# Kernel tuning notes

Measured on AMD Instinct MI355X. Metric: run time of the kernel, lower is better.

The kernel has to match this reference:

```python
import jax, jax.numpy as jnp
import numpy as np

B, S, N_CATE, N_CONT = 32, 1024, 4, 4
HIDDEN, ATTN, VOCAB, EMB = 1024, 512, 1000, 128


def sinusoidal_pe(seq_len, d_model, base=10000.0):
    pos = jnp.arange(seq_len, dtype=jnp.float32)[:, None]            # [S,1]
    i = jnp.arange(d_model // 2, dtype=jnp.float32)[None, :]         # [1,D/2]
    ang = pos / jnp.power(base, 2.0 * i / d_model)                   # [S,D/2]
    pe = jnp.zeros((seq_len, d_model), dtype=jnp.float32)
    pe = pe.at[:, 0::2].set(jnp.sin(ang))
    pe = pe.at[:, 1::2].set(jnp.cos(ang))
    return pe


def setup_inputs() -> dict:
    key = jax.random.key(0)
    ks = jax.random.split(key, 20)
    s = 0.02
    inp = {
        "cate_x": jax.random.randint(ks[0], (B, S, N_CATE), 0, VOCAB, dtype=jnp.int64)
                  if jax.config.read("jax_enable_x64") else
                  jax.random.randint(ks[0], (B, S, N_CATE), 0, VOCAB, dtype=jnp.int32),
        "cont_x": jax.random.normal(ks[1], (B, S, N_CONT), dtype=jnp.float32),
        "mask": jnp.ones((B, S), dtype=bool),
        "targets": jax.random.uniform(ks[2], (B, S), dtype=jnp.float32),
        # EntireEmbedding params: 4 cate tables + cont linear + comb projection
        "E0": jax.random.normal(ks[3], (VOCAB, EMB), dtype=jnp.float32) * s,
        "E1": jax.random.normal(ks[4], (VOCAB, EMB), dtype=jnp.float32) * s,
        "E2": jax.random.normal(ks[5], (VOCAB, EMB), dtype=jnp.float32) * s,
        "E3": jax.random.normal(ks[6], (VOCAB, EMB), dtype=jnp.float32) * s,
        "Wc": jax.random.normal(ks[7], (N_CONT, N_CATE * EMB), dtype=jnp.float32) * s,
        "Wproj": jax.random.normal(ks[8], (2 * N_CATE * EMB, HIDDEN), dtype=jnp.float32) * s,
        # two-head attention linears (bias=False)
        "WQ1": jax.random.normal(ks[9], (HIDDEN, ATTN), dtype=jnp.float32) * s,
        "WK1": jax.random.normal(ks[10], (HIDDEN, ATTN), dtype=jnp.float32) * s,
        "WV1": jax.random.normal(ks[11], (HIDDEN, ATTN), dtype=jnp.float32) * s,
        "WQ2": jax.random.normal(ks[12], (HIDDEN, ATTN), dtype=jnp.float32) * s,
        "WK2": jax.random.normal(ks[13], (HIDDEN, ATTN), dtype=jnp.float32) * s,
        "WV2": jax.random.normal(ks[14], (HIDDEN, ATTN), dtype=jnp.float32) * s,
        "W0": jax.random.normal(ks[15], (2 * ATTN, HIDDEN), dtype=jnp.float32) * s,
        "Wf": jax.random.normal(ks[16], (HIDDEN, 1), dtype=jnp.float32) * s,
    }
    return inp


def _attend(x, WQ, WK, WV):
    Q = x @ WQ  # [B,S,A]
    K = x @ WK
    V = x @ WV
    scores = jnp.einsum("bqd,bkd->bqk", Q, K) / jnp.sqrt(jnp.float32(ATTN))
    # faithful to nn.Softmax(dim=1): normalize over the QUERY axis
    attn = jax.nn.softmax(scores, axis=1)
    return jnp.einsum("bqk,bkv->bqv", attn, V)


def reference(cate_x, cont_x, mask, targets, E0, E1, E2, E3, Wc, Wproj,
              WQ1, WK1, WV1, WQ2, WK2, WV2, W0, Wf):
    # EntireEmbedding: per-feature cate embeddings + cont projection -> comb proj
    cate_emb = jnp.concatenate(
        [E0[cate_x[..., 0]], E1[cate_x[..., 1]], E2[cate_x[..., 2]], E3[cate_x[..., 3]]],
        axis=-1)                                   # [B,S,512]
    cont_emb = cont_x @ Wc                          # [B,S,512]
    x = jnp.concatenate([cate_emb, cont_emb], axis=-1) @ Wproj  # [B,S,H]
    x = x + sinusoidal_pe(x.shape[1], HIDDEN)[None, :, :]
    z1 = _attend(x, WQ1, WK1, WV1)                  # [B,S,A]
    z2 = _attend(x, WQ2, WK2, WV2)                  # [B,S,A]
    z = jnp.concatenate([z1, z2], axis=-1) @ W0     # [B,S,H]
    out = jax.nn.sigmoid(z @ Wf)                    # FinalConnecting: Linear(H,1)+sigmoid
    return out.squeeze(-1)                          # [B,S]
```

## Files before the change

kernel.cpp:

```cpp
#include <hip/hip_runtime.h>
#include <hip/hip_bf16.h>
#include <math.h>

#define BB    32
#define SS    1024
#define HID   1024
#define AT    512
#define NVOC  1000
#define NT    (BB*SS)

typedef unsigned short u16;
typedef __attribute__((ext_vector_type(8))) short s16x8;
typedef __attribute__((ext_vector_type(4))) float f32x4;

__device__ __forceinline__ float bf2f(u16 u) {
    union { unsigned int i; float f; } x; x.i = ((unsigned int)u) << 16; return x.f;
}
__device__ __forceinline__ u16 f2bf(float f) {
    union { float f; unsigned int i; } u; u.f = f;
    unsigned int r = u.i + 0x7fffu + ((u.i >> 16) & 1u);
    return (u16)(r >> 16);
}
__device__ __forceinline__ float4 ld4(const float* p) { return *(const float4*)p; }
__device__ __forceinline__ float4 ld4bf(const u16* p) {
    ushort4 v = *(const ushort4*)p;
    return make_float4(bf2f(v.x), bf2f(v.y), bf2f(v.z), bf2f(v.w));
}

__device__ __forceinline__ void gld16(const u16* g, u16* l) {
    __builtin_amdgcn_global_load_lds(
        (const __attribute__((address_space(1))) unsigned int*)g,
        (__attribute__((address_space(3))) unsigned int*)l,
        16, 0, 0);
}

struct Ptrs4f { const float* p[4]; };

__device__ __forceinline__ float blockReduceSum(float x) {
    #pragma unroll
    for (int off = 32; off > 0; off >>= 1) x += __shfl_down(x, off, 64);
    __shared__ float tmp[4];
    int lane = threadIdx.x & 63, wid = threadIdx.x >> 6;
    if (lane == 0) tmp[wid] = x;
    __syncthreads();
    if (threadIdx.x == 0) x = tmp[0] + tmp[1] + tmp[2] + tmp[3];
    return x;
}
__device__ __forceinline__ float waveReduceSum(float x) {
    #pragma unroll
    for (int off = 32; off > 0; off >>= 1) x += __shfl_down(x, off, 64);
    return x;
}

__global__ void k_prep(Ptrs4f E, const float* __restrict__ Wproj,
                       u16* __restrict__ PE16, u16* __restrict__ E16o, u16* __restrict__ Wp16) {
    int blk = blockIdx.x, tid = threadIdx.x;
    if (blk < 2048) {
        int idx = blk*256 + tid;
        int s = idx >> 9, i = idx & 511;
        const float l2_10000 = 13.287712379549449f;
        float denom = exp2f((2.f * (float)i / 1024.f) * l2_10000);
        float ang = (float)s / denom;
        unsigned int pack = ((unsigned int)f2bf(cosf(ang)) << 16) | f2bf(sinf(ang));
        *(unsigned int*)(PE16 + (size_t)s*1024 + 2*i) = pack;
    } else if (blk < 4048) {
        int id2 = blk - 2048;
        int f = id2 / 500;
        int i = (id2 % 500)*256 + tid;
        E16o[(size_t)f*128000 + i] = f2bf(E.p[f][i]);
    } else {
        int i = (blk - 4048)*256 + tid;
        Wp16[i] = f2bf(Wproj[i]);
    }
}

__global__ void k_transp(Ptrs4f src, u16* __restrict__ dst, int R, int C) {
    const float* in = src.p[blockIdx.z];
    u16* out = dst + (size_t)blockIdx.z * R * C;
    int r0 = blockIdx.y*32, c0 = blockIdx.x*32;
    __shared__ float tt[32][33];
    tt[threadIdx.y][threadIdx.x] = in[(size_t)(r0 + threadIdx.y)*C + c0 + threadIdx.x];
    __syncthreads();
    out[(size_t)(c0 + threadIdx.y)*R + r0 + threadIdx.x] = f2bf(tt[threadIdx.x][threadIdx.y]);
}

__global__ void k_pre1(const float* __restrict__ W0, const float* __restrict__ Wf,
                       const float* __restrict__ Wc, const float* __restrict__ Wproj,
                       float* __restrict__ W0f, float* __restrict__ Wcp, float* __restrict__ CQ) {
    int blk = blockIdx.x, tid = threadIdx.x;
    if (blk < 1024) {
        const float* row = W0 + (size_t)blk*1024;
        float a = 0.f;
        for (int j = tid; j < 1024; j += 256) a += row[j] * Wf[j];
        a = blockReduceSum(a);
        if (tid == 0) W0f[blk] = a;
    } else if (blk < 1040) {
        int r = blk - 1024; int c = r >> 2, is = r & 3; int i = is*256 + tid;
        float a = 0.f;
        for (int j = 0; j < 512; ++j) a += Wc[c*512 + j] * Wproj[(size_t)(512 + j)*1024 + i];
        Wcp[c*1024 + i] = a;
    } else {
        int r = blk - 1040;
        CQ[r*256 + tid] = 0.f;
    }
}

__global__ void k_pre2(Ptrs4f W, const float* __restrict__ WV1, const float* __restrict__ WV2,
                       const float* __restrict__ W0f, const float* __restrict__ Wcp,
                       float* __restrict__ v, float* __restrict__ CQ) {
    int blk = blockIdx.x, tid = threadIdx.x;
    if (blk < 2048) {
        int h = blk >> 10, i = blk & 1023;
        const float* WV = h ? WV2 : WV1;
        const float* wf = W0f + h*512;
        float a = 0.f;
        for (int aa = tid; aa < 512; aa += 256) a += WV[(size_t)i*512 + aa] * wf[aa];
        a = blockReduceSum(a);
        if (tid == 0) v[h*1024 + i] = a;
    } else {
        int r = blk - 2048;
        int ns = r & 1, wc = (r >> 1) & 15, jc = r >> 5;
        int w = wc & 3, c = wc >> 2; int n = ns*256 + tid;
        const float* Ww = W.p[w];
        float a = 0.f;
        for (int j = jc*128; j < jc*128 + 128; ++j) a += Wcp[c*1024 + j] * Ww[(size_t)j*512 + n];
        atomicAdd(&CQ[(size_t)(w*4 + c)*512 + n], a);
    }
}

__device__ __forceinline__ void cstore(float* p, float v) { *p = v; }
__device__ __forceinline__ void cstore(u16* p, float v)   { *p = f2bf(v); }

template<typename CT, bool STATS, bool CTRANS>
__device__ __forceinline__ void mfma_gemm(const u16* __restrict__ A, const u16* __restrict__ B,
                                          CT* __restrict__ C, int M, int N, int K, float alpha,
                                          float* __restrict__ Pm, float* __restrict__ Pd,
                                          int m0, int n0) {
    __shared__ u16 As[128*64];
    __shared__ u16 Bs[128*64];
    const int tid = threadIdx.x;
    const int wave = tid >> 6, lane = tid & 63;
    const int quad = lane >> 4, l16 = lane & 15;
    const int wm = (wave >> 1)*64, wn = (wave & 1)*64;
    const int srow = lane >> 3;
    const int scol = ((lane & 7) ^ srow) * 8;
    f32x4 acc[4][4] = {};

    for (int k0 = 0; k0 < K; k0 += 64) {
        #pragma unroll
        for (int p = 0; p < 4; ++p) {
            int rb = wave*32 + p*8;
            gld16(A + (size_t)(m0 + rb + srow)*K + k0 + scol, As + rb*64);
            gld16(B + (size_t)(n0 + rb + srow)*K + k0 + scol, Bs + rb*64);
        }
        __syncthreads();
        #pragma unroll
        for (int kk = 0; kk < 2; ++kk) {
            s16x8 af[4], bf[4];
            #pragma unroll
            for (int i = 0; i < 4; ++i) {
                int row = wm + i*16 + l16;
                af[i] = *(const s16x8*)(As + row*64 + (((kk*4 + quad) ^ (row & 7)) * 8));
            }
            #pragma unroll
            for (int j = 0; j < 4; ++j) {
                int row = wn + j*16 + l16;
                bf[j] = *(const s16x8*)(Bs + row*64 + (((kk*4 + quad) ^ (row & 7)) * 8));
            }
            #pragma unroll
            for (int i = 0; i < 4; ++i)
                #pragma unroll
                for (int j = 0; j < 4; ++j)
                    acc[i][j] = __builtin_amdgcn_mfma_f32_16x16x32_bf16(af[i], bf[j], acc[i][j], 0, 0, 0);
        }
        __syncthreads();
    }
    if (STATS) {
        #pragma unroll
        for (int i = 0; i < 4; ++i)
            #pragma unroll
            for (int r = 0; r < 4; ++r) {
                int gm = m0 + wm + i*16 + quad*4 + r;
                u16 b0 = f2bf(acc[i][0][r] * alpha);
                u16 b1 = f2bf(acc[i][1][r] * alpha);
                u16 b2 = f2bf(acc[i][2][r] * alpha);
                u16 b3 = f2bf(acc[i][3][r] * alpha);
                acc[i][0][r] = bf2f(b0); acc[i][1][r] = bf2f(b1);
                acc[i][2][r] = bf2f(b2); acc[i][3][r] = bf2f(b3);
                unsigned int lo = (unsigned int)b0 | ((unsigned int)b1 << 16);
                unsigned int hi = (unsigned int)b2 | ((unsigned int)b3 << 16);
                *(uint2*)((u16*)C + (size_t)gm*N + n0 + wn + l16*4) = make_uint2(lo, hi);
            }
        __shared__ float sMax[4][64];
        __shared__ float sSum[4][64];
        #pragma unroll
        for (int j = 0; j < 4; ++j) {
            float mx = -3.4e38f;
            #pragma unroll
            for (int i = 0; i < 4; ++i)
                #pragma unroll
                for (int r = 0; r < 4; ++r) mx = fmaxf(mx, acc[i][j][r]);
            mx = fmaxf(mx, __shfl_xor(mx, 16, 64));
            mx = fmaxf(mx, __shfl_xor(mx, 32, 64));
            float sm = 0.f;
            #pragma unroll
            for (int i = 0; i < 4; ++i)
                #pragma unroll
                for (int r = 0; r < 4; ++r) sm += exp2f(acc[i][j][r] - mx);
            sm += __shfl_xor(sm, 16, 64);
            sm += __shfl_xor(sm, 32, 64);
            if (quad == 0) { sMax[wave][j*16 + l16] = mx; sSum[wave][j*16 + l16] = sm; }
        }
        __syncthreads();
        if (tid < 128) {
            int c = tid;
            int w0 = (c < 64) ? 0 : 1, ci = c & 63;
            float m0v = sMax[w0][ci],     s0 = sSum[w0][ci];
            float m1v = sMax[w0 + 2][ci], s1 = sSum[w0 + 2][ci];
            float mm = fmaxf(m0v, m1v);
            float ss = s0 * exp2f(m0v - mm) + s1 * exp2f(m1v - mm);
            Pm[n0 + c] = mm;
            Pd[n0 + c] = ss;
        }
    } else {
        #pragma unroll
        for (int i = 0; i < 4; ++i) {
            #pragma unroll
            for (int r = 0; r < 4; ++r) {
                int gm = m0 + wm + i*16 + quad*4 + r;
                if (gm < M) {
                    #pragma unroll
                    for (int j = 0; j < 4; ++j) {
                        int gn = n0 + wn + j*16 + l16;
                        if (CTRANS) cstore(C + (size_t)gn*M + gm, acc[i][j][r] * alpha);
                        else        cstore(C + (size_t)gm*N + gn, acc[i][j][r] * alpha);
                    }
                }
            }
        }
    }
}

__global__ __launch_bounds__(256) void k_pw_pre3(const u16* __restrict__ Wp16, const u16* __restrict__ Wt,
                                                 u16* __restrict__ PWT,
                                                 const float* __restrict__ Wproj, const float* __restrict__ v,
                                                 float* __restrict__ pv) {
    int blk = blockIdx.x;
    if (blk < 64) {
        int x = blk & 3, z = blk >> 2;
        int f = z >> 2, w = z & 3;
        mfma_gemm<u16,false,true>(Wp16 + (size_t)f*128*1024, Wt + (size_t)w*512*1024,
                                  PWT + (size_t)z*512*128, 128, 512, 1024, 1.f,
                                  nullptr, nullptr, 0, x*128);
    } else {
        int b2 = blk - 64, tid = threadIdx.x;
        int i = b2 & 127, fh = b2 >> 7; int f = fh >> 1, h = fh & 1;
        const float* row = Wproj + (size_t)(f*128 + i)*1024;
        const float* vh = v + h*1024;
        float a = 0.f;
        for (int j = tid; j < 1024; j += 256) a += row[j] * vh[j];
        a = blockReduceSum(a);
        if (tid == 0) pv[(size_t)fh*128 + i] = a;
    }
}

__global__ __launch_bounds__(256) void k_g_TP(const u16* __restrict__ E16, const u16* __restrict__ PWT,
                                              const u16* __restrict__ PE16, const u16* __restrict__ Wt,
                                              u16* __restrict__ TQK16, u16* __restrict__ PEQ16) {
    int z = blockIdx.z;
    if (z < 16) {
        int f = z >> 2;
        mfma_gemm<u16,false,false>(E16 + (size_t)f*128000, PWT + (size_t)z*512*128,
                   TQK16 + (size_t)z*1000*512, 1000, 512, 128, 1.f, nullptr, nullptr,
                   blockIdx.y*128, blockIdx.x*128);
    } else {
        int w = z - 16;
        mfma_gemm<u16,false,false>(PE16, Wt + (size_t)w*512*1024, PEQ16 + (size_t)w*1024*512,
                   1024, 512, 1024, 1.f, nullptr, nullptr, blockIdx.y*128, blockIdx.x*128);
    }
}

__global__ __launch_bounds__(256, 6) void k_g_S(const u16* __restrict__ Q, const u16* __restrict__ K,
                                             u16* __restrict__ Sb, float alpha,
                                             float* __restrict__ Pm, float* __restrict__ Pd, int b0) {
    size_t b = blockIdx.z;
    int bx = (blockIdx.x % 4)*2 + (blockIdx.y % 2);
    int by = (blockIdx.x / 4)*4 + (blockIdx.y / 2);
    size_t po = ((b0 + b)*8 + by)*1024;
    mfma_gemm<u16,true,false>(Q + b*SS*AT, K + b*SS*AT, Sb + b*SS*SS, 1024, 1024, 512, alpha,
                        Pm + po, Pd + po, by*128, bx*128);
}

__global__ void k_dots(const u16* __restrict__ E16, const u16* __restrict__ PE16,
                       const float* __restrict__ Wcp, const float* __restrict__ v,
                       const float* __restrict__ pv,
                       float* __restrict__ Ut, float* __restrict__ pu, float* __restrict__ cu) {
    int id = blockIdx.x;
    if (id < 2000) {
        int wave = threadIdx.x >> 6, lane = threadIdx.x & 63;
        int d = id*4 + wave;
        int f = d / 2000, h = (d / 1000) & 1, r = d % 1000;
        unsigned int e2 = *(const unsigned int*)(E16 + ((size_t)f*1000 + r)*128 + lane*2);
        const float* pvp = pv + (size_t)(f*2 + h)*128 + lane*2;
        float a = bf2f((u16)(e2 & 0xffff)) * pvp[0] + bf2f((u16)(e2 >> 16)) * pvp[1];
        a = waveReduceSum(a);
        if (lane == 0) Ut[(size_t)(f*2 + h)*1000 + r] = a;
    } else if (id < 4048) {
        int tq = id - 2000; int h = tq >> 10, s = tq & 1023;
        float4 a = ld4bf(PE16 + (size_t)s*1024 + threadIdx.x*4);
        float4 b = ld4(v + h*1024 + threadIdx.x*4);
        float p = a.x*b.x + a.y*b.y + a.z*b.z + a.w*b.w;
        p = blockReduceSum(p);
        if (threadIdx.x == 0) pu[h*1024 + s] = p;
    } else {
        int tq = id - 4048; int h = tq >> 2, c = tq & 3;
        float4 a = ld4(Wcp + c*1024 + threadIdx.x*4);
        float4 b = ld4(v + h*1024 + threadIdx.x*4);
        float p = a.x*b.x + a.y*b.y + a.z*b.z + a.w*b.w;
        p = blockReduceSum(p);
        if (threadIdx.x == 0) cu[h*4 + c] = p;
    }
}

__device__ __forceinline__ void unpack8(uint4 v, float* x) {
    x[0] = bf2f((u16)(v.x & 0xffff)); x[1] = bf2f((u16)(v.x >> 16));
    x[2] = bf2f((u16)(v.y & 0xffff)); x[3] = bf2f((u16)(v.y >> 16));
    x[4] = bf2f((u16)(v.z & 0xffff)); x[5] = bf2f((u16)(v.z >> 16));
    x[6] = bf2f((u16)(v.w & 0xffff)); x[7] = bf2f((u16)(v.w >> 16));
}

__global__ void k_gather(const int* __restrict__ cate, const float* __restrict__ cont,
                         const u16* __restrict__ TQK, const float* __restrict__ CQ,
                         const u16* __restrict__ PEQ, const float* __restrict__ Ut,
                         const float* __restrict__ cu, const float* __restrict__ pu,
                         u16* __restrict__ Qh, u16* __restrict__ Kh,
                         float* __restrict__ u, int h) {
    int tid = threadIdx.x;
    size_t t = (size_t)blockIdx.x*2 + (tid >> 7);
    int r = tid & 127;
    int s = (int)(t & 1023);
    int4 cc = *(const int4*)(cate + t*4);
    float4 cv = ld4(cont + t*4);
    int e = r >> 6;
    int w = 2*h + e;
    int n = (r & 63)*8;
    const u16* t0 = TQK + ((size_t)(0*4  + w)*1000 + cc.x)*512 + n;
    const u16* t1 = TQK + ((size_t)(1*4  + w)*1000 + cc.y)*512 + n;
    const u16* t2 = TQK + ((size_t)(2*4  + w)*1000 + cc.z)*512 + n;
    const u16* t3 = TQK + ((size_t)(3*4  + w)*1000 + cc.w)*512 + n;
    const u16* pq = PEQ + ((size_t)w*1024 + s)*512 + n;
    const float* cq = CQ + (size_t)w*2048 + n;
    float a0[8], a1[8], a2[8], a3[8], ap[8];
    unpack8(*(const uint4*)t0, a0); unpack8(*(const uint4*)t1, a1);
    unpack8(*(const uint4*)t2, a2); unpack8(*(const uint4*)t3, a3);
    unpack8(*(const uint4*)pq, ap);
    unsigned int pack[4];
    #pragma unroll
    for (int jp = 0; jp < 4; ++jp) {
        float x0, x1;
        #pragma unroll
        for (int half = 0; half < 2; ++half) {
            int j = jp*2 + half;
            float x = a0[j] + a1[j] + a2[j] + a3[j] + ap[j]
                    + cv.x*cq[j] + cv.y*cq[512+j] + cv.z*cq[1024+j] + cv.w*cq[1536+j];
            if (half == 0) x0 = x; else x1 = x;
        }
        pack[jp] = ((unsigned int)f2bf(x1) << 16) | f2bf(x0);
    }
    u16* op = (e ? Kh : Qh) + t*512 + n;
    *(uint4*)op = make_uint4(pack[0], pack[1], pack[2], pack[3]);
    if (r == 0) {
        float uu = pu[h*1024 + s]
                 + Ut[(0*2 + h)*1000 + cc.x] + Ut[(1*2 + h)*1000 + cc.y]
                 + Ut[(2*2 + h)*1000 + cc.z] + Ut[(3*2 + h)*1000 + cc.w]
                 + cv.x*cu[h*4+0] + cv.y*cu[h*4+1] + cv.z*cu[h*4+2] + cv.w*cu[h*4+3];
        u[(size_t)h*NT + t] = uu;
    }
}

__global__ void k_stats_combine(const float* __restrict__ Pm, const float* __restrict__ Pd,
                                const float* __restrict__ u, float* __restrict__ wexp, int b0) {
    int idx = b0*1024 + blockIdx.x*256 + threadIdx.x;
    int b = idx >> 10, k = idx & 1023;
    float mx = -3.4e38f;
    #pragma unroll
    for (int mt = 0; mt < 8; ++mt) mx = fmaxf(mx, Pm[((size_t)b*8 + mt)*1024 + k]);
    float dd = 0.f;
    #pragma unroll
    for (int mt = 0; mt < 8; ++mt) dd += Pd[((size_t)b*8 + mt)*1024 + k]
                                       * exp2f(Pm[((size_t)b*8 + mt)*1024 + k] - mx);
    int q = (k & ~63) | (((k & 15) << 2) | ((k & 63) >> 4));
    wexp[((size_t)b << 10) + q] = u[idx] / dd * exp2f(-mx);
}

__global__ void k_logit(const u16* __restrict__ Sb, const float* __restrict__ wexp,
                        float* __restrict__ logits, int b0, int init) {
    int wave = threadIdx.x >> 6, lane = threadIdx.x & 63;
    size_t tl = (size_t)blockIdx.x*4 + wave;
    size_t tabs = (size_t)b0*1024 + tl;
    int b = (int)(tabs >> 10);
    const u16* row = Sb + tl*1024;
    const float* wb = wexp + ((size_t)b << 10);
    float acc = 0.f;
    #pragma unroll
    for (int half = 0; half < 2; ++half) {
        int k = lane*8 + half*512;
        float4 s0 = ld4bf(row + k), s1 = ld4bf(row + k + 4);
        float4 w0 = ld4(wb + k),    w1 = ld4(wb + k + 4);
        acc += exp2f(s0.x)*w0.x + exp2f(s0.y)*w0.y + exp2f(s0.z)*w0.z + exp2f(s0.w)*w0.w
             + exp2f(s1.x)*w1.x + exp2f(s1.y)*w1.y + exp2f(s1.z)*w1.z + exp2f(s1.w)*w1.w;
    }
    acc = waveReduceSum(acc);
    if (lane == 0) { if (init) logits[tabs] = acc; else logits[tabs] += acc; }
}

__global__ void k_final(const float* __restrict__ logits, float* __restrict__ out) {
    int t = blockIdx.x*256 + threadIdx.x;
    float x = logits[t];
    out[t] = 1.f / (1.f + expf(-x));
}

extern "C" void kernel_launch(void* const* d_in, const int* in_sizes, int n_in,
                              void* d_out, int out_size, void* d_ws, size_t ws_size,
                              hipStream_t stream) {
    const int*   cate = (const int*)d_in[0];
    const float* cont = (const float*)d_in[1];
    Ptrs4f E; E.p[0] = (const float*)d_in[4]; E.p[1] = (const float*)d_in[5];
              E.p[2] = (const float*)d_in[6]; E.p[3] = (const float*)d_in[7];
    const float* Wc    = (const float*)d_in[8];
    const float* Wproj = (const float*)d_in[9];
    Ptrs4f W; W.p[0] = (const float*)d_in[10];
              W.p[1] = (const float*)d_in[11];
              W.p[2] = (const float*)d_in[13];
              W.p[3] = (const float*)d_in[14];
    const float* WV1 = (const float*)d_in[12];
    const float* WV2 = (const float*)d_in[15];
    const float* W0  = (const float*)d_in[16];
    const float* Wf  = (const float*)d_in[17];

    char* base = (char*)d_ws;
    size_t off = 0;
    auto alloc = [&](size_t bytes) { void* p = base + off; off += (bytes + 255) & ~(size_t)255; return p; };
    u16*   PE16  = (u16*)  alloc(1048576ull*2);
    u16*   E16   = (u16*)  alloc(4ull*1000*128*2);
    u16*   Wt    = (u16*)  alloc(4ull*512*1024*2);
    u16*   Wp16  = (u16*)  alloc(512ull*1024*2);
    u16*   PWT   = (u16*)  alloc(16ull*512*128*2);
    u16*   TQK16 = (u16*)  alloc(16ull*1000*512*2);
    u16*   PEQ16 = (u16*)  alloc(4ull*1024*512*2);
    float* Wcp   = (float*)alloc(4*1024*4);
    float* W0f   = (float*)alloc(1024*4);
    float* vv    = (float*)alloc(2*1024*4);
    float* CQ    = (float*)alloc(16*512*4);
    float* pvb   = (float*)alloc(8*128*4);
    float* Ut    = (float*)alloc(8*1000*4);
    float* cu    = (float*)alloc(8*4);
    float* pu    = (float*)alloc(2*1024*4);
    float* ubuf  = (float*)alloc(2ull*NT*4);
    u16*   Qh    = (u16*)  alloc((size_t)NT*512*2);
    u16*   Kh    = (u16*)  alloc((size_t)NT*512*2);
    float* Pm    = (float*)alloc(32ull*8*1024*4);
    float* Pd    = (float*)alloc(32ull*8*1024*4);
    float* wbuf  = (float*)alloc(32*1024*4);
    float* logits= (float*)alloc((size_t)NT*4);
    size_t sChunkBytes = (size_t)SS*SS*2;
    size_t remain = (ws_size > off) ? (ws_size - off) : 0;
    int NB = (int)(remain / sChunkBytes);
    if (NB > 32) NB = 32;
    if (NB < 1) NB = 1;
    u16* Sbuf = (u16*)(base + off);

    const float alpha = 0.06375954951107036f;

    k_prep<<<6096, 256, 0, stream>>>(E, Wproj, PE16, E16, Wp16);
    k_transp<<<dim3(16, 32, 4), dim3(32, 32), 0, stream>>>(W, Wt, 1024, 512);
    k_pre1<<<1072, 256, 0, stream>>>(W0, Wf, Wc, Wproj, W0f, Wcp, CQ);
    k_pre2<<<2304, 256, 0, stream>>>(W, WV1, WV2, W0f, Wcp, vv, CQ);
    k_pw_pre3<<<1088, 256, 0, stream>>>(Wp16, Wt, PWT, Wproj, vv, pvb);
    k_g_TP<<<dim3(4, 8, 20), 256, 0, stream>>>(E16, PWT, PE16, Wt, TQK16, PEQ16);
    k_dots<<<4056, 256, 0, stream>>>(E16, PE16, Wcp, vv, pvb, Ut, pu, cu);

    for (int h = 0; h < 2; ++h) {
        k_gather<<<NT/2, 256, 0, stream>>>(cate, cont, TQK16, CQ, PEQ16, Ut, cu, pu, Qh, Kh, ubuf, h);
        for (int b0 = 0; b0 < 32; b0 += NB) {
            int nb = (32 - b0 < NB) ? (32 - b0) : NB;
            k_g_S<<<dim3(8, 8, nb), 256, 0, stream>>>(Qh + (size_t)b0*SS*AT, Kh + (size_t)b0*SS*AT, Sbuf, alpha, Pm, Pd, b0);
            k_stats_combine<<<nb*4, 256, 0, stream>>>(Pm, Pd, ubuf + (size_t)h*NT, wbuf, b0);
            k_logit<<<nb*256, 256, 0, stream>>>(Sbuf, wbuf, logits, b0, h == 0 ? 1 : 0);
        }
    }
    k_final<<<128, 256, 0, stream>>>(logits, (float*)d_out);
}
```

Measured before the change: 393.1 us.

## Merge preprocessing kernels into four stages and fuse final sigmoid into logit

Collapses the seven weight-preprocessing launches into four multi-role kernels, reorganized by dependency stage: the transpose and W0·Wf go into stage 1, the Wc·Wproj product is split across blocks with atomics, and the CQ computation moves to stage 3. The separate final sigmoid kernel is folded into the second-head logit pass. k_logit also walks blocks in reverse order, likely to reuse recently written S chunks in cache, and loads bf16 values with a single 16-byte load. This removes launch overhead and a pass over the logits, at the cost of more complex block dispatch and extra atomics.

```diff
diff --git a/kernel.cpp b/kernel.cpp
--- a/kernel.cpp
+++ b/kernel.cpp
@@ -25,6 +25,12 @@
 __device__ __forceinline__ float4 ld4bf(const u16* p) {
     ushort4 v = *(const ushort4*)p;
     return make_float4(bf2f(v.x), bf2f(v.y), bf2f(v.z), bf2f(v.w));
+}
+__device__ __forceinline__ void unpack8(uint4 v, float* x) {
+    x[0] = bf2f((u16)(v.x & 0xffff)); x[1] = bf2f((u16)(v.x >> 16));
+    x[2] = bf2f((u16)(v.y & 0xffff)); x[3] = bf2f((u16)(v.y >> 16));
+    x[4] = bf2f((u16)(v.z & 0xffff)); x[5] = bf2f((u16)(v.z >> 16));
+    x[6] = bf2f((u16)(v.w & 0xffff)); x[7] = bf2f((u16)(v.w >> 16));
 }
 
 __device__ __forceinline__ void gld16(const u16* g, u16* l) {
@@ -52,8 +58,11 @@
     return x;
 }
 
-__global__ void k_prep(Ptrs4f E, const float* __restrict__ Wproj,
-                       u16* __restrict__ PE16, u16* __restrict__ E16o, u16* __restrict__ Wp16) {
+__global__ void k_s1(Ptrs4f E, const float* __restrict__ Wproj, Ptrs4f W,
+                     const float* __restrict__ W0, const float* __restrict__ Wf,
+                     u16* __restrict__ PE16, u16* __restrict__ E16o, u16* __restrict__ Wp16,
+                     u16* __restrict__ Wt, float* __restrict__ W0f,
+                     float* __restrict__ Wcp, float* __restrict__ CQ) {
     int blk = blockIdx.x, tid = threadIdx.x;
     if (blk < 2048) {
         int idx = blk*256 + tid;
@@ -68,63 +77,59 @@
         int f = id2 / 500;
         int i = (id2 % 500)*256 + tid;
         E16o[(size_t)f*128000 + i] = f2bf(E.p[f][i]);
-    } else {
+    } else if (blk < 6096) {
         int i = (blk - 4048)*256 + tid;
         Wp16[i] = f2bf(Wproj[i]);
-    }
-}
-
-__global__ void k_transp(Ptrs4f src, u16* __restrict__ dst, int R, int C) {
-    const float* in = src.p[blockIdx.z];
-    u16* out = dst + (size_t)blockIdx.z * R * C;
-    int r0 = blockIdx.y*32, c0 = blockIdx.x*32;
-    __shared__ float tt[32][33];
-    tt[threadIdx.y][threadIdx.x] = in[(size_t)(r0 + threadIdx.y)*C + c0 + threadIdx.x];
-    __syncthreads();
-    out[(size_t)(c0 + threadIdx.y)*R + r0 + threadIdx.x] = f2bf(tt[threadIdx.x][threadIdx.y]);
-}
-
-__global__ void k_pre1(const float* __restrict__ W0, const float* __restrict__ Wf,
-                       const float* __restrict__ Wc, const float* __restrict__ Wproj,
-                       float* __restrict__ W0f, float* __restrict__ Wcp, float* __restrict__ CQ) {
+    } else if (blk < 8144) {
+        int tb = blk - 6096;
+        int mat = tb >> 9, t2 = tb & 511;
+        int cx = t2 & 15, ry = t2 >> 4;
+        int r0 = ry*32, c0 = cx*32;
+        const float* in = W.p[mat];
+        u16* out = Wt + (size_t)mat*1024*512;
+        __shared__ float tt[32][33];
+        int tx = tid & 31, ty8 = tid >> 5;
+        #pragma unroll
+        for (int it = 0; it < 4; ++it)
+            tt[ty8 + it*8][tx] = in[(size_t)(r0 + ty8 + it*8)*512 + c0 + tx];
+        __syncthreads();
+        #pragma unroll
+        for (int it = 0; it < 4; ++it)
+            out[(size_t)(c0 + ty8 + it*8)*1024 + r0 + tx] = f2bf(tt[tx][ty8 + it*8]);
+    } else if (blk < 9168) {
+        int row = blk - 8144;
+        const float* rp = W0 + (size_t)row*1024;
+        float a = 0.f;
+        for (int j = tid; j < 1024; j += 256) a += rp[j] * Wf[j];
+        a = blockReduceSum(a);
+        if (tid == 0) W0f[row] = a;
+    } else {
+        int idx = (blk - 9168)*256 + tid;
+        if (idx < 4096) Wcp[idx] = 0.f;
+        else CQ[idx - 4096] = 0.f;
+    }
+}
+
+__global__ void k_s2(const float* __restrict__ Wc, const float* __restrict__ Wproj,
+                     Ptrs4f W, const float* __restrict__ WV1, const float* __restrict__ WV2,
+                     const float* __restrict__ W0f, float* __restrict__ Wcp, float* __restrict__ v) {
     int blk = blockIdx.x, tid = threadIdx.x;
-    if (blk < 1024) {
-        const float* row = W0 + (size_t)blk*1024;
+    if (blk < 64) {
+        int c = blk >> 4, ic = (blk >> 2) & 3, jc = blk & 3;
+        int i = ic*256 + tid;
         float a = 0.f;
-        for (int j = tid; j < 1024; j += 256) a += row[j] * Wf[j];
-        a = blockReduceSum(a);
-        if (tid == 0) W0f[blk] = a;
-    } else if (blk < 1040) {
-        int r = blk - 1024; int c = r >> 2, is = r & 3; int i = is*256 + tid;
-        float a = 0.f;
-        for (int j = 0; j < 512; ++j) a += Wc[c*512 + j] * Wproj[(size_t)(512 + j)*1024 + i];
-        Wcp[c*1024 + i] = a;
+        for (int j = jc*128; j < jc*128 + 128; ++j)
+            a += Wc[c*512 + j] * Wproj[(size_t)(512 + j)*1024 + i];
+        atomicAdd(&Wcp[c*1024 + i], a);
     } else {
-        int r = blk - 1040;
-        CQ[r*256 + tid] = 0.f;
-    }
-}
-
-__global__ void k_pre2(Ptrs4f W, const float* __restrict__ WV1, const float* __restrict__ WV2,
-                       const float* __restrict__ W0f, const float* __restrict__ Wcp,
-                       float* __restrict__ v, float* __restrict__ CQ) {
-    int blk = blockIdx.x, tid = threadIdx.x;
-    if (blk < 2048) {
-        int h = blk >> 10, i = blk & 1023;
+        int b2 = blk - 64;
+        int h = b2 >> 10, i = b2 & 1023;
         const float* WV = h ? WV2 : WV1;
         const float* wf = W0f + h*512;
         float a = 0.f;
         for (int aa = tid; aa < 512; aa += 256) a += WV[(size_t)i*512 + aa] * wf[aa];
         a = blockReduceSum(a);
         if (tid == 0) v[h*1024 + i] = a;
-    } else {
-        int r = blk - 2048;
-        int ns = r & 1, wc = (r >> 1) & 15, jc = r >> 5;
-        int w = wc & 3, c = wc >> 2; int n = ns*256 + tid;
-        const float* Ww = W.p[w];
-        float a = 0.f;
-        for (int j = jc*128; j < jc*128 + 128; ++j) a += Wcp[c*1024 + j] * Ww[(size_t)j*512 + n];
-        atomicAdd(&CQ[(size_t)(w*4 + c)*512 + n], a);
     }
 }
 
@@ -241,19 +246,28 @@
     }
 }
 
-__global__ __launch_bounds__(256) void k_pw_pre3(const u16* __restrict__ Wp16, const u16* __restrict__ Wt,
-                                                 u16* __restrict__ PWT,
-                                                 const float* __restrict__ Wproj, const float* __restrict__ v,
-                                                 float* __restrict__ pv) {
-    int blk = blockIdx.x;
+__global__ __launch_bounds__(256) void k_s3(const u16* __restrict__ Wp16, const u16* __restrict__ Wt,
+                                            u16* __restrict__ PWT,
+                                            Ptrs4f W, const float* __restrict__ Wcp, float* __restrict__ CQ,
+                                            const float* __restrict__ Wproj, const float* __restrict__ v,
+                                            float* __restrict__ pv) {
+    int blk = blockIdx.x, tid = threadIdx.x;
     if (blk < 64) {
         int x = blk & 3, z = blk >> 2;
         int f = z >> 2, w = z & 3;
         mfma_gemm<u16,false,true>(Wp16 + (size_t)f*128*1024, Wt + (size_t)w*512*1024,
                                   PWT + (size_t)z*512*128, 128, 512, 1024, 1.f,
                                   nullptr, nullptr, 0, x*128);
+    } else if (blk < 320) {
+        int r = blk - 64;
+        int ns = r & 1, wc = (r >> 1) & 15, jc = r >> 5;
+        int w = wc & 3, c = wc >> 2; int n = ns*256 + tid;
+        const float* Ww = W.p[w];
+        float a = 0.f;
+        for (int j = jc*128; j < jc*128 + 128; ++j) a += Wcp[c*1024 + j] * Ww[(size_t)j*512 + n];
+        atomicAdd(&CQ[(size_t)(w*4 + c)*512 + n], a);
     } else {
-        int b2 = blk - 64, tid = threadIdx.x;
+        int b2 = blk - 320;
         int i = b2 & 127, fh = b2 >> 7; int f = fh >> 1, h = fh & 1;
         const float* row = Wproj + (size_t)(f*128 + i)*1024;
         const float* vh = v + h*1024;
@@ -264,38 +278,28 @@
     }
 }
 
-__global__ __launch_bounds__(256) void k_g_TP(const u16* __restrict__ E16, const u16* __restrict__ PWT,
-                                              const u16* __restrict__ PE16, const u16* __restrict__ Wt,
-                                              u16* __restrict__ TQK16, u16* __restrict__ PEQ16) {
-    int z = blockIdx.z;
-    if (z < 16) {
-        int f = z >> 2;
-        mfma_gemm<u16,false,false>(E16 + (size_t)f*128000, PWT + (size_t)z*512*128,
-                   TQK16 + (size_t)z*1000*512, 1000, 512, 128, 1.f, nullptr, nullptr,
-                   blockIdx.y*128, blockIdx.x*128);
-    } else {
-        int w = z - 16;
-        mfma_gemm<u16,false,false>(PE16, Wt + (size_t)w*512*1024, PEQ16 + (size_t)w*1024*512,
-                   1024, 512, 1024, 1.f, nullptr, nullptr, blockIdx.y*128, blockIdx.x*128);
-    }
-}
-
-__global__ __launch_bounds__(256, 6) void k_g_S(const u16* __restrict__ Q, const u16* __restrict__ K,
-                                             u16* __restrict__ Sb, float alpha,
-                                             float* __restrict__ Pm, float* __restrict__ Pd, int b0) {
-    size_t b = blockIdx.z;
-    int bx = (blockIdx.x % 4)*2 + (blockIdx.y % 2);
-    int by = (blockIdx.x / 4)*4 + (blockIdx.y / 2);
-    size_t po = ((b0 + b)*8 + by)*1024;
-    mfma_gemm<u16,true,false>(Q + b*SS*AT, K + b*SS*AT, Sb + b*SS*SS, 1024, 1024, 512, alpha,
-                        Pm + po, Pd + po, by*128, bx*128);
-}
-
-__global__ void k_dots(const u16* __restrict__ E16, const u16* __restrict__ PE16,
-                       const float* __restrict__ Wcp, const float* __restrict__ v,
-                       const float* __restrict__ pv,
-                       float* __restrict__ Ut, float* __restrict__ pu, float* __restrict__ cu) {
-    int id = blockIdx.x;
+__global__ __launch_bounds__(256) void k_s4(const u16* __restrict__ E16, const u16* __restrict__ PWT,
+                                            const u16* __restrict__ PE16, const u16* __restrict__ Wt,
+                                            u16* __restrict__ TQK16, u16* __restrict__ PEQ16,
+                                            const float* __restrict__ Wcp, const float* __restrict__ v,
+                                            const float* __restrict__ pv,
+                                            float* __restrict__ Ut, float* __restrict__ pu, float* __restrict__ cu) {
+    int blk = blockIdx.x;
+    if (blk < 640) {
+        int z = blk >> 5, r = blk & 31, y = r >> 2, x = r & 3;
+        if (z < 16) {
+            int f = z >> 2;
+            mfma_gemm<u16,false,false>(E16 + (size_t)f*128000, PWT + (size_t)z*512*128,
+                       TQK16 + (size_t)z*1000*512, 1000, 512, 128, 1.f, nullptr, nullptr,
+                       y*128, x*128);
+        } else {
+            int w = z - 16;
+            mfma_gemm<u16,false,false>(PE16, Wt + (size_t)w*512*1024, PEQ16 + (size_t)w*1024*512,
+                       1024, 512, 1024, 1.f, nullptr, nullptr, y*128, x*128);
+        }
+        return;
+    }
+    int id = blk - 640;
     if (id < 2000) {
         int wave = threadIdx.x >> 6, lane = threadIdx.x & 63;
         int d = id*4 + wave;
@@ -322,11 +326,15 @@
     }
 }
 
-__device__ __forceinline__ void unpack8(uint4 v, float* x) {
-    x[0] = bf2f((u16)(v.x & 0xffff)); x[1] = bf2f((u16)(v.x >> 16));
-    x[2] = bf2f((u16)(v.y & 0xffff)); x[3] = bf2f((u16)(v.y >> 16));
-    x[4] = bf2f((u16)(v.z & 0xffff)); x[5] = bf2f((u16)(v.z >> 16));
-    x[6] = bf2f((u16)(v.w & 0xffff)); x[7] = bf2f((u16)(v.w >> 16));
+__global__ __launch_bounds__(256, 6) void k_g_S(const u16* __restrict__ Q, const u16* __restrict__ K,
+                                             u16* __restrict__ Sb, float alpha,
+                                             float* __restrict__ Pm, float* __restrict__ Pd, int b0) {
+    size_t b = blockIdx.z;
+    int bx = (blockIdx.x % 4)*2 + (blockIdx.y % 2);
+    int by = (blockIdx.x / 4)*4 + (blockIdx.y / 2);
+    size_t po = ((b0 + b)*8 + by)*1024;
+    mfma_gemm<u16,true,false>(Q + b*SS*AT, K + b*SS*AT, Sb + b*SS*SS, 1024, 1024, 512, alpha,
+                        Pm + po, Pd + po, by*128, bx*128);
 }
 
 __global__ void k_gather(const int* __restrict__ cate, const float* __restrict__ cont,
@@ -394,9 +402,11 @@
 }
 
 __global__ void k_logit(const u16* __restrict__ Sb, const float* __restrict__ wexp,
-                        float* __restrict__ logits, int b0, int init) {
+                        float* __restrict__ logits, float* __restrict__ out,
+                        int b0, int mode) {
     int wave = threadIdx.x >> 6, lane = threadIdx.x & 63;
-    size_t tl = (size_t)blockIdx.x*4 + wave;
+    size_t bi = (size_t)(gridDim.x - 1 - blockIdx.x);
+    size_t tl = bi*4 + wave;
     size_t tabs = (size_t)b0*1024 + tl;
     int b = (int)(tabs >> 10);
     const u16* row = Sb + tl*1024;
@@ -405,19 +415,20 @@
     #pragma unroll
     for (int half = 0; half < 2; ++half) {
         int k = lane*8 + half*512;
-        float4 s0 = ld4bf(row + k), s1 = ld4bf(row + k + 4);
-        float4 w0 = ld4(wb + k),    w1 = ld4(wb + k + 4);
-        acc += exp2f(s0.x)*w0.x + exp2f(s0.y)*w0.y + exp2f(s0.z)*w0.z + exp2f(s0.w)*w0.w
-             + exp2f(s1.x)*w1.x + exp2f(s1.y)*w1.y + exp2f(s1.z)*w1.z + exp2f(s1.w)*w1.w;
+        float sv[8];
+        unpack8(*(const uint4*)(row + k), sv);
+        float4 w0 = ld4(wb + k), w1 = ld4(wb + k + 4);
+        acc += exp2f(sv[0])*w0.x + exp2f(sv[1])*w0.y + exp2f(sv[2])*w0.z + exp2f(sv[3])*w0.w
+             + exp2f(sv[4])*w1.x + exp2f(sv[5])*w1.y + exp2f(sv[6])*w1.z + exp2f(sv[7])*w1.w;
     }
     acc = waveReduceSum(acc);
-    if (lane == 0) { if (init) logits[tabs] = acc; else logits[tabs] += acc; }
-}
-
-__global__ void k_final(const float* __restrict__ logits, float* __restrict__ out) {
-    int t = blockIdx.x*256 + threadIdx.x;
-    float x = logits[t];
-    out[t] = 1.f / (1.f + expf(-x));
+    if (lane == 0) {
+        if (mode == 0) logits[tabs] = acc;
+        else {
+            float x = logits[tabs] + acc;
+            out[tabs] = 1.f / (1.f + expf(-x));
+        }
+    }
 }
 
 extern "C" void kernel_launch(void* const* d_in, const int* in_sizes, int n_in,
@@ -472,13 +483,10 @@
 
     const float alpha = 0.06375954951107036f;
 
-    k_prep<<<6096, 256, 0, stream>>>(E, Wproj, PE16, E16, Wp16);
-    k_transp<<<dim3(16, 32, 4), dim3(32, 32), 0, stream>>>(W, Wt, 1024, 512);
-    k_pre1<<<1072, 256, 0, stream>>>(W0, Wf, Wc, Wproj, W0f, Wcp, CQ);
-    k_pre2<<<2304, 256, 0, stream>>>(W, WV1, WV2, W0f, Wcp, vv, CQ);
-    k_pw_pre3<<<1088, 256, 0, stream>>>(Wp16, Wt, PWT, Wproj, vv, pvb);
-    k_g_TP<<<dim3(4, 8, 20), 256, 0, stream>>>(E16, PWT, PE16, Wt, TQK16, PEQ16);
-    k_dots<<<4056, 256, 0, stream>>>(E16, PE16, Wcp, vv, pvb, Ut, pu, cu);
+    k_s1<<<9216, 256, 0, stream>>>(E, Wproj, W, W0, Wf, PE16, E16, Wp16, Wt, W0f, Wcp, CQ);
+    k_s2<<<2112, 256, 0, stream>>>(Wc, Wproj, W, WV1, WV2, W0f, Wcp, vv);
+    k_s3<<<1344, 256, 0, stream>>>(Wp16, Wt, PWT, W, Wcp, CQ, Wproj, vv, pvb);
+    k_s4<<<4696, 256, 0, stream>>>(E16, PWT, PE16, Wt, TQK16, PEQ16, Wcp, vv, pvb, Ut, pu, cu);
 
     for (int h = 0; h < 2; ++h) {
         k_gather<<<NT/2, 256, 0, stream>>>(cate, cont, TQK16, CQ, PEQ16, Ut, cu, pu, Qh, Kh, ubuf, h);
@@ -486,8 +494,7 @@
             int nb = (32 - b0 < NB) ? (32 - b0) : NB;
             k_g_S<<<dim3(8, 8, nb), 256, 0, stream>>>(Qh + (size_t)b0*SS*AT, Kh + (size_t)b0*SS*AT, Sbuf, alpha, Pm, Pd, b0);
             k_stats_combine<<<nb*4, 256, 0, stream>>>(Pm, Pd, ubuf + (size_t)h*NT, wbuf, b0);
-            k_logit<<<nb*256, 256, 0, stream>>>(Sbuf, wbuf, logits, b0, h == 0 ? 1 : 0);
-        }
-    }
-    k_final<<<128, 256, 0, stream>>>(logits, (float*)d_out);
-}
+            k_logit<<<nb*256, 256, 0, stream>>>(Sbuf, wbuf, logits, (float*)d_out, b0, h);
+        }
+    }
+}
```

Measured after the change: 367.1 us. -6.6%, faster.
